# Kernel optimization log

Measured on AMD Instinct MI355X. Metric: run time of the kernel, lower is better.

## Reference

```python
import jax, jax.numpy as jnp
import numpy as np

L = 5  # number of attention+MLP stages

def _layernorm(x, g, b, eps=1e-5):
    mu = x.mean(-1, keepdims=True)
    var = ((x - mu) ** 2).mean(-1, keepdims=True)
    return (x - mu) * jax.lax.rsqrt(var + eps) * g + b

def setup_inputs() -> dict:
    key = jax.random.key(0)
    B, N, C = 8, 2048, 512  # win_size=4, num_slices=12 -> C = 4*4*384//12 = 512
    ks = jax.random.split(key, 7)
    s = 0.02
    return {
        "x": jax.random.normal(ks[0], (B, N, C), dtype=jnp.float32),
        "qkv_w": jax.random.normal(ks[1], (L, C, 3 * C), dtype=jnp.float32) * s,
        "qkv_b": jnp.zeros((L, 3 * C), dtype=jnp.float32),
        "ln_g": jnp.ones((L, C), dtype=jnp.float32),
        "ln_b": jnp.zeros((L, C), dtype=jnp.float32),
        "fc1_w": jax.random.normal(ks[2], (L, C, 2 * C), dtype=jnp.float32) * s,
        "fc1_b": jnp.zeros((L, 2 * C), dtype=jnp.float32),
        "fc2_w": jax.random.normal(ks[3], (L, 2 * C, C), dtype=jnp.float32) * s,
        "fc2_b": jnp.zeros((L, C), dtype=jnp.float32),
    }

def reference(x, qkv_w, qkv_b, ln_g, ln_b, fc1_w, fc1_b, fc2_w, fc2_b):
    B, N, C = x.shape
    half = N // 2
    scale = C ** -0.5  # num_heads = 1 -> head_dim = C
    # Custom block mask: top-left (half x half) block fully visible,
    # top-right block masked; bottom half is tril with diagonal = N//2,
    # i.e. global row i >= half may attend to columns j <= i.
    i = jnp.arange(N)[:, None]
    j = jnp.arange(N)[None, :]
    allowed = jnp.where(i < half, j < half, j <= i)
    bias = jnp.where(allowed, 0.0, -1000.0).astype(x.dtype)  # (N, N)
    for l in range(L):
        # Mask3dAttention (single head)
        qkv = x @ qkv_w[l] + qkv_b[l]                      # (B, N, 3C)
        q, k, v = jnp.split(qkv, 3, axis=-1)               # each (B, N, C)
        attn = jnp.einsum("bnc,bmc->bnm", q * scale, k) + bias
        attn = jax.nn.softmax(attn, axis=-1)
        x = jnp.einsum("bnm,bmc->bnc", attn, v)
        # residual MLP on normed features
        y = _layernorm(x, ln_g[l], ln_b[l])
        h = jax.nn.gelu(y @ fc1_w[l] + fc1_b[l], approximate=False)
        x = x + (h @ fc2_w[l] + fc2_b[l])
    return x
```

## Files before the change

### kernel.cpp

```cpp
#include <hip/hip_runtime.h>
#include <math.h>

typedef unsigned short u16;
typedef __attribute__((ext_vector_type(8))) short bf16x8;
typedef __attribute__((ext_vector_type(4))) float f32x4;
typedef __attribute__((ext_vector_type(4))) unsigned short u16x4;

#define NLAYERS 5
#define BATCH 8
#define SEQ 2048
#define CH 512
#define ROWS_TOTAL (BATCH * SEQ)
#define HALF (SEQ / 2)
#define QSCALE_EXP2 0.06375871529f
#define EXP2_CAP 86.56f

#define SMEM_U16 32768

__device__ __forceinline__ u16 f2bf(float f) {
    unsigned u = __float_as_uint(f);
    u += 0x7fffu + ((u >> 16) & 1u);
    return (u16)(u >> 16);
}

__device__ __forceinline__ unsigned pk2(float a, float b) {
    unsigned r;
    asm("v_cvt_pk_bf16_f32 %0, %1, %2" : "=v"(r) : "v"(a), "v"(b));
    return r;
}

__device__ __forceinline__ u16x4 pack4(f32x4 v) {
    union { unsigned u[2]; u16x4 o; } r;
    r.u[0] = pk2(v[0], v[1]);
    r.u[1] = pk2(v[2], v[3]);
    return r.o;
}

__device__ __forceinline__ void st16(u16* p, u16x4 v) { *(u16x4*)p = v; }
__device__ __forceinline__ void st16f(float* p, f32x4 v) { *(f32x4*)p = v; }

__device__ __forceinline__ float fexp2(float x) {
    float r;
    asm("v_exp_f32 %0, %1" : "=v"(r) : "v"(x));
    return r;
}

__device__ __forceinline__ void llds16(const u16* g, u16* l) {
    __builtin_amdgcn_global_load_lds(
        (const __attribute__((address_space(1))) unsigned int*)g,
        (__attribute__((address_space(3))) unsigned int*)l, 16, 0, 0);
}

__device__ __forceinline__ void xcd_rc(int& rt, int& ct) {
    const int n = blockIdx.x;
    const int m = n >> 3;
    rt = (n & 7) * 16 + (m & 15);
    ct = m >> 4;
}

__device__ __forceinline__ void mm_issue(const u16* gA, const u16* gB,
                                         u16* lA, u16* lB, int lda, int ldb)
{
#pragma unroll
    for (int i = 0; i < 4; ++i)
        llds16(gA + (size_t)i * 32 * lda, lA + i * 2048);
#pragma unroll
    for (int i = 0; i < 4; ++i)
        llds16(gB + (size_t)i * 32 * ldb, lB + i * 2048);
}

__device__ __forceinline__ void mm_compute(const u16* As, const u16* Bs,
                                           const int aoff[2][4],
                                           const int boff[2][4],
                                           f32x4 acc[4][4])
{
#pragma unroll
    for (int h = 0; h < 2; ++h) {
        bf16x8 af[4], bfv[4];
#pragma unroll
        for (int t = 0; t < 4; ++t) af[t]  = *(const bf16x8*)&As[aoff[h][t]];
#pragma unroll
        for (int t = 0; t < 4; ++t) bfv[t] = *(const bf16x8*)&Bs[boff[h][t]];
#pragma unroll
        for (int ti = 0; ti < 4; ++ti)
#pragma unroll
            for (int tj = 0; tj < 4; ++tj)
                acc[ti][tj] = __builtin_amdgcn_mfma_f32_16x16x32_bf16(
                    af[ti], bfv[tj], acc[ti][tj], 0, 0, 0);
    }
}

__device__ __forceinline__ void mm_core(
    const u16* __restrict__ A, int lda,
    const u16* __restrict__ Bt, int ldb,
    int row0, int col0, int K,
    u16* SM, f32x4 acc[4][4])
{
    const int tid  = threadIdx.x;
    const int wave = tid >> 6, lane = tid & 63;
    const int wm = (wave & 1) * 64, wn = (wave >> 1) * 64;
    const int q  = lane >> 4,  ln = lane & 15;

    const int sr8 = lane >> 3;
    const int sc  = (lane & 7) ^ sr8;
    const u16* gA = A  + (size_t)(row0 + wave * 8 + sr8) * lda + sc * 8;
    const u16* gB = Bt + (size_t)(col0 + wave * 8 + sr8) * ldb + sc * 8;

    u16* const A0 = SM;
    u16* const B0 = SM + 8192;
    u16* const A1 = SM + 16384;
    u16* const B1 = SM + 24576;
    u16* const w0a = A0 + wave * 512;
    u16* const w0b = B0 + wave * 512;
    u16* const w1a = A1 + wave * 512;
    u16* const w1b = B1 + wave * 512;

    int aoff[2][4], boff[2][4];
#pragma unroll
    for (int h = 0; h < 2; ++h) {
        const int pos = (((h * 4 + q) ^ (ln & 7)) * 8);
#pragma unroll
        for (int t = 0; t < 4; ++t) {
            aoff[h][t] = (wm + t * 16 + ln) * 64 + pos;
            boff[h][t] = (wn + t * 16 + ln) * 64 + pos;
        }
    }

#pragma unroll
    for (int ti = 0; ti < 4; ++ti)
#pragma unroll
        for (int tj = 0; tj < 4; ++tj)
#pragma unroll
            for (int e = 0; e < 4; ++e) acc[ti][tj][e] = 0.f;

    mm_issue(gA, gB, w0a, w0b, lda, ldb);
    gA += 64; gB += 64;

    for (int k0 = 0; k0 < K; k0 += 128) {
        if (k0 + 64 < K) {
            mm_issue(gA, gB, w1a, w1b, lda, ldb);
            gA += 64; gB += 64;
            asm volatile("s_waitcnt vmcnt(8)" ::: "memory");
        } else {
            asm volatile("s_waitcnt vmcnt(0)" ::: "memory");
        }
        __builtin_amdgcn_s_barrier();
        mm_compute(A0, B0, aoff, boff, acc);
        __builtin_amdgcn_s_barrier();
        __builtin_amdgcn_sched_barrier(0);
        if (k0 + 128 < K) {
            mm_issue(gA, gB, w0a, w0b, lda, ldb);
            gA += 64; gB += 64;
            asm volatile("s_waitcnt vmcnt(8)" ::: "memory");
        } else {
            asm volatile("s_waitcnt vmcnt(0)" ::: "memory");
        }
        __builtin_amdgcn_s_barrier();
        mm_compute(A1, B1, aoff, boff, acc);
        __builtin_amdgcn_s_barrier();
        __builtin_amdgcn_sched_barrier(0);
    }
}

template <typename F>
__device__ __forceinline__ void epi_emit(f32x4 acc[4][4], float* eb, F emit)
{
    const int tid = threadIdx.x, wave = tid >> 6, lane = tid & 63;
    const int wn = (wave >> 1) * 64;
    const int q = lane >> 4, ln = lane & 15;
#pragma unroll
    for (int p = 0; p < 4; ++p) {
        __syncthreads();
        if ((wave & 1) == (p >> 1)) {
            const int tibase = (p & 1) * 2;
#pragma unroll
            for (int tj = 0; tj < 4; ++tj)
#pragma unroll
                for (int t2 = 0; t2 < 2; ++t2)
#pragma unroll
                    for (int r = 0; r < 4; ++r)
                        eb[(t2 * 16 + q * 4 + r) * 132 + wn + tj * 16 + ln] =
                            acc[tibase + t2][tj][r];
        }
        __syncthreads();
#pragma unroll
        for (int s = 0; s < 4; ++s) {
            const int row = s * 8 + (tid >> 5);
            const int col = (tid & 31) * 4;
            f32x4 v = *(const f32x4*)&eb[row * 132 + col];
            emit(p * 32 + row, col, v);
        }
    }
}

__global__ __launch_bounds__(256) void qkv_gemm(
    const u16* __restrict__ A, const u16* __restrict__ Bt,
    const float* __restrict__ bias,
    u16* __restrict__ Qb, u16* __restrict__ Kb, u16* __restrict__ Vt,
    float* __restrict__ rowsum)
{
    __shared__ __align__(16) u16 SMEM[SMEM_U16];
    f32x4 acc[4][4];
    int rt, ct; xcd_rc(rt, ct);
    const int row0 = rt * 128, col0 = ct * 128;
    if (ct == 0 && threadIdx.x < 128)
        rowsum[row0 + threadIdx.x] = 0.f;
    mm_core(A, CH, Bt, CH, row0, col0, CH, SMEM, acc);

    if (ct < 8) {
        u16* dst = (ct < 4) ? Qb : Kb;
        const int cbase = (ct < 4) ? col0 : col0 - CH;
        const float sc = (ct < 4) ? QSCALE_EXP2 : 1.0f;
        epi_emit(acc, (float*)SMEM, [&](int row, int col, f32x4 v) {
            const float4 bb = *(const float4*)&bias[col0 + col];
            v[0] = (v[0] + bb.x) * sc; v[1] = (v[1] + bb.y) * sc;
            v[2] = (v[2] + bb.z) * sc; v[3] = (v[3] + bb.w) * sc;
            st16(&dst[(size_t)(row0 + row) * CH + cbase + col], pack4(v));
        });
    } else {
        const int tid = threadIdx.x, wave = tid >> 6, lane = tid & 63;
        const int wm = (wave & 1) * 64, wn = (wave >> 1) * 64;
        const int q = lane >> 4, ln = lane & 15;
#pragma unroll
        for (int tj = 0; tj < 4; ++tj) {
            const int gcol = col0 + wn + tj * 16 + ln;
            const float bv = bias[gcol];
#pragma unroll
            for (int ti = 0; ti < 4; ++ti) {
                const int grow = row0 + wm + ti * 16 + q * 4;
                const int b = grow >> 11, j = grow & (SEQ - 1);
                f32x4 vv;
                vv[0] = acc[ti][tj][0] + bv; vv[1] = acc[ti][tj][1] + bv;
                vv[2] = acc[ti][tj][2] + bv; vv[3] = acc[ti][tj][3] + bv;
                st16(&Vt[(size_t)b * CH * SEQ +
                         (size_t)(gcol - 2 * CH) * SEQ + j], pack4(vv));
            }
        }
    }
}

__global__ __launch_bounds__(256) void qk_gemm(
    const u16* __restrict__ Qb, const u16* __restrict__ Kb,
    u16* __restrict__ Sb, float* __restrict__ rowsum)
{
    const int id = blockIdx.x;
    const int b = id & 7, jt = (id >> 3) & 15, it = id >> 7;
    if (it < 8) { if (jt >= 8) return; } else if (jt > it) return;
    __shared__ __align__(16) u16 SMEM[SMEM_U16];
    f32x4 acc[4][4];
    const u16* A  = Qb + (size_t)b * SEQ * CH;
    const u16* Bt = Kb + (size_t)b * SEQ * CH;
    u16* S = Sb + (size_t)b * SEQ * SEQ;
    const int row0 = it * 128, col0 = jt * 128;
    mm_core(A, CH, Bt, CH, row0, col0, CH, SMEM, acc);

    const bool upper = (it < 8);
    const int tid = threadIdx.x;
    epi_emit(acc, (float*)SMEM, [&](int row, int col, f32x4 v) {
        const int grow = row0 + row;
        const int gcol = col0 + col;
        f32x4 pv;
#pragma unroll
        for (int e = 0; e < 4; ++e) {
            const bool allowed = upper || (gcol + e <= grow);
            pv[e] = allowed ? fexp2(fminf(v[e], EXP2_CAP)) : 0.f;
        }
        st16(&S[(size_t)grow * SEQ + gcol], pack4(pv));
        float rs = pv[0] + pv[1] + pv[2] + pv[3];
        rs += __shfl_xor(rs, 1, 64);
        rs += __shfl_xor(rs, 2, 64);
        rs += __shfl_xor(rs, 4, 64);
        rs += __shfl_xor(rs, 8, 64);
        rs += __shfl_xor(rs, 16, 64);
        if ((tid & 31) == 0)
            atomicAdd(&rowsum[b * SEQ + grow], rs);
    });
}

__global__ __launch_bounds__(256) void pv_gemm(
    const u16* __restrict__ Sb, const u16* __restrict__ Vt,
    const float* __restrict__ rowsum, float* __restrict__ O)
{
    const int n = blockIdx.x;
    const int b = n & 7, m = n >> 3;
    const int it = 15 - (m >> 2), ct = m & 3;
    const int Kfull = ((it < 8) ? 8 : (it + 1)) * 128;
    __shared__ __align__(16) u16 SMEM[SMEM_U16];
    f32x4 acc[4][4];
    const u16* A  = Sb + (size_t)b * SEQ * SEQ;
    const u16* Bt = Vt + (size_t)b * CH * SEQ;
    const int row0 = it * 128, col0 = ct * 128;
    mm_core(A, SEQ, Bt, SEQ, row0, col0, Kfull, SMEM, acc);

    epi_emit(acc, (float*)SMEM, [&](int row, int col, f32x4 v) {
        const int grow = row0 + row;
        const float rden = 1.0f / rowsum[b * SEQ + grow];
        v[0] *= rden; v[1] *= rden; v[2] *= rden; v[3] *= rden;
        st16f(&O[(size_t)(b * SEQ + grow) * CH + col0 + col], v);
    });
}

__global__ __launch_bounds__(256) void fc1_gemm(
    const u16* __restrict__ A, const u16* __restrict__ Bt,
    const float* __restrict__ bias, u16* __restrict__ H)
{
    __shared__ __align__(16) u16 SMEM[SMEM_U16];
    f32x4 acc[4][4];
    int rt, ct; xcd_rc(rt, ct);
    const int row0 = rt * 128, col0 = ct * 128;
    mm_core(A, CH, Bt, CH, row0, col0, CH, SMEM, acc);
    epi_emit(acc, (float*)SMEM, [&](int row, int col, f32x4 v) {
        const float4 bb = *(const float4*)&bias[col0 + col];
        v[0] += bb.x; v[1] += bb.y; v[2] += bb.z; v[3] += bb.w;
#pragma unroll
        for (int e = 0; e < 4; ++e)
            v[e] = 0.5f * v[e] * (1.f + erff(v[e] * 0.70710678118654752f));
        st16(&H[(size_t)(row0 + row) * (2 * CH) + col0 + col], pack4(v));
    });
}

template <bool WRITE_X>
__global__ __launch_bounds__(256) void fc2_gemm(
    const u16* __restrict__ A, const u16* __restrict__ Bt,
    const float* __restrict__ bias, float* __restrict__ X,
    u16* __restrict__ Xb)
{
    __shared__ __align__(16) u16 SMEM[SMEM_U16];
    f32x4 acc[4][4];
    int rt, ct; xcd_rc(rt, ct);
    const int row0 = rt * 128, col0 = ct * 128;
    mm_core(A, 2 * CH, Bt, 2 * CH, row0, col0, 2 * CH, SMEM, acc);
    epi_emit(acc, (float*)SMEM, [&](int row, int col, f32x4 v) {
        const size_t idx = (size_t)(row0 + row) * CH + col0 + col;
        const float4 bb = *(const float4*)&bias[col0 + col];
        const f32x4 xv = *(const f32x4*)&X[idx];
        v[0] += bb.x + xv[0]; v[1] += bb.y + xv[1];
        v[2] += bb.z + xv[2]; v[3] += bb.w + xv[3];
        if (WRITE_X) st16f(&X[idx], v);
        st16(&Xb[idx], pack4(v));
    });
}

__device__ __forceinline__ float block_sum(float v, volatile float* red, int tid)
{
#pragma unroll
    for (int off = 1; off < 64; off <<= 1) v += __shfl_xor(v, off, 64);
    __syncthreads();
    if ((tid & 63) == 0) red[tid >> 6] = v;
    __syncthreads();
    return red[0] + red[1] + red[2] + red[3];
}

__global__ __launch_bounds__(256) void ln_kernel(
    const float* __restrict__ x, const float* __restrict__ g,
    const float* __restrict__ bta, u16* __restrict__ y)
{
    __shared__ float red[4];
    const int tid = threadIdx.x;
    const size_t base = (size_t)blockIdx.x * CH;
    float x0 = x[base + tid];
    float x1 = x[base + 256 + tid];
    float mu = block_sum(x0 + x1, red, tid) * (1.f / CH);
    float d0 = x0 - mu, d1 = x1 - mu;
    float var = block_sum(d0 * d0 + d1 * d1, red, tid) * (1.f / CH);
    float w = 1.f / sqrtf(var + 1e-5f);
    const float y0 = d0 * w * g[tid]       + bta[tid];
    const float y1 = d1 * w * g[256 + tid] + bta[256 + tid];
    const unsigned pk = pk2(y0, y1);
    y[base + tid]       = (u16)(pk & 0xffffu);
    y[base + 256 + tid] = (u16)(pk >> 16);
}

__global__ __launch_bounds__(256) void f2bf_kernel(
    const float* __restrict__ in, u16* __restrict__ out)
{
    const int i = blockIdx.x * 256 + threadIdx.x;
    float4 vv = ((const float4*)in)[i];
    f32x4 v; v[0] = vv.x; v[1] = vv.y; v[2] = vv.z; v[3] = vv.w;
    u16x4 o = pack4(v);
    *(u16x4*)&out[(size_t)i * 4] = o;
}

__global__ __launch_bounds__(256) void wtrans_kernel(
    const float* __restrict__ in, u16* __restrict__ out, int K, int N)
{
    __shared__ float tile[32][33];
    const int l = blockIdx.z;
    in  += (size_t)l * K * N;
    out += (size_t)l * K * N;
    const int n0 = blockIdx.x * 32, k0 = blockIdx.y * 32;
    const int r = threadIdx.x >> 3, c4 = (threadIdx.x & 7) * 4;
    float4 v = *(const float4*)&in[(size_t)(k0 + r) * N + n0 + c4];
    tile[r][c4 + 0] = v.x; tile[r][c4 + 1] = v.y;
    tile[r][c4 + 2] = v.z; tile[r][c4 + 3] = v.w;
    __syncthreads();
    f32x4 t;
    t[0] = tile[c4 + 0][r]; t[1] = tile[c4 + 1][r];
    t[2] = tile[c4 + 2][r]; t[3] = tile[c4 + 3][r];
    st16(&out[(size_t)(n0 + r) * K + k0 + c4], pack4(t));
}

extern "C" void kernel_launch(void* const* d_in, const int* in_sizes, int n_in,
                              void* d_out, int out_size, void* d_ws, size_t ws_size,
                              hipStream_t stream)
{
    const float* x_in  = (const float*)d_in[0];
    const float* qkv_w = (const float*)d_in[1];
    const float* qkv_b = (const float*)d_in[2];
    const float* ln_g  = (const float*)d_in[3];
    const float* ln_b  = (const float*)d_in[4];
    const float* fc1_w = (const float*)d_in[5];
    const float* fc1_b = (const float*)d_in[6];
    const float* fc2_w = (const float*)d_in[7];
    const float* fc2_b = (const float*)d_in[8];

    float* xbuf = (float*)d_out;

    char* p = (char*)d_ws;
    u16* qkv_wt = (u16*)p; p += (size_t)NLAYERS * 1536 * 512 * 2;
    u16* fc1_wt = (u16*)p; p += (size_t)NLAYERS * 1024 * 512 * 2;
    u16* fc2_wt = (u16*)p; p += (size_t)NLAYERS * 512 * 1024 * 2;
    u16* xb = (u16*)p; p += (size_t)ROWS_TOTAL * CH * 2;
    u16* Qb = (u16*)p; p += (size_t)ROWS_TOTAL * CH * 2;
    u16* Kb = (u16*)p; p += (size_t)ROWS_TOTAL * CH * 2;
    u16* Vt = (u16*)p; p += (size_t)ROWS_TOTAL * CH * 2;
    float* rowsum = (float*)p; p += (size_t)ROWS_TOTAL * 4;
    u16* Sb = (u16*)p;
    u16* yb = Sb;
    u16* hb = Sb + (size_t)ROWS_TOTAL * CH;

    const dim3 blk(256);

    f2bf_kernel<<<dim3(ROWS_TOTAL * CH / 1024), blk, 0, stream>>>(x_in, xb);
    wtrans_kernel<<<dim3(1536 / 32, 512 / 32, NLAYERS), blk, 0, stream>>>(
        qkv_w, qkv_wt, 512, 1536);
    wtrans_kernel<<<dim3(1024 / 32, 512 / 32, NLAYERS), blk, 0, stream>>>(
        fc1_w, fc1_wt, 512, 1024);
    wtrans_kernel<<<dim3(512 / 32, 1024 / 32, NLAYERS), blk, 0, stream>>>(
        fc2_w, fc2_wt, 1024, 512);

    for (int l = 0; l < NLAYERS; ++l) {
        qkv_gemm<<<dim3(128 * 12), blk, 0, stream>>>(
            xb, qkv_wt + (size_t)l * 1536 * 512, qkv_b + (size_t)l * 1536,
            Qb, Kb, Vt, rowsum);
        qk_gemm<<<dim3(2048), blk, 0, stream>>>(Qb, Kb, Sb, rowsum);
        pv_gemm<<<dim3(512), blk, 0, stream>>>(Sb, Vt, rowsum, xbuf);
        ln_kernel<<<dim3(ROWS_TOTAL), blk, 0, stream>>>(
            xbuf, ln_g + (size_t)l * CH, ln_b + (size_t)l * CH, yb);
        fc1_gemm<<<dim3(128 * 8), blk, 0, stream>>>(
            yb, fc1_wt + (size_t)l * 1024 * 512, fc1_b + (size_t)l * 1024, hb);
        if (l < NLAYERS - 1)
            fc2_gemm<false><<<dim3(128 * 4), blk, 0, stream>>>(
                hb, fc2_wt + (size_t)l * 512 * 1024, fc2_b + (size_t)l * 512,
                xbuf, xb);
        else
            fc2_gemm<true><<<dim3(128 * 4), blk, 0, stream>>>(
                hb, fc2_wt + (size_t)l * 512 * 1024, fc2_b + (size_t)l * 512,
                xbuf, xb);
    }
}
```

Baseline: 1.045 ms.

## Retile QK^T GEMM to 128x256 tiles with 512 threads and compact grid

Replaces the QK score kernel with a 512-thread variant computing 128x256 output tiles, so each Q tile load is reused across twice as many key columns. The grid is compacted to enumerate only the needed tiles of the block-causal mask instead of launching 2048 blocks and early-exiting most of them. The epilogue is staged through shared memory in four 32-row passes to fit the smaller LDS budget, with a full-wave rowsum reduction. Some tiles at the causal boundary now cover partially masked columns, which adds wasted work there, and the larger block with 4 blocks per CU may raise register pressure.

Measured after the change: 980.5 us. 6.2% less time.

```diff
diff --git a/kernel.cpp b/kernel.cpp
--- a/kernel.cpp
+++ b/kernel.cpp
@@ -16,6 +16,7 @@
 #define EXP2_CAP 86.56f
 
 #define SMEM_U16 32768
+#define QK2_U16 24576
 
 __device__ __forceinline__ u16 f2bf(float f) {
     unsigned u = __float_as_uint(f);
@@ -239,42 +240,116 @@
     }
 }
 
-__global__ __launch_bounds__(256) void qk_gemm(
+__global__ __launch_bounds__(512, 4) void qk2_gemm(
     const u16* __restrict__ Qb, const u16* __restrict__ Kb,
     u16* __restrict__ Sb, float* __restrict__ rowsum)
 {
+    __shared__ __align__(16) u16 SMEM[QK2_U16];
+    u16* const As = SMEM;
+    u16* const Bs = SMEM + 8192;
+    float* const eb = (float*)SMEM;
+
     const int id = blockIdx.x;
-    const int b = id & 7, jt = (id >> 3) & 15, it = id >> 7;
-    if (it < 8) { if (jt >= 8) return; } else if (jt > it) return;
-    __shared__ __align__(16) u16 SMEM[SMEM_U16];
+    const int b = id & 7;
+    int u = id >> 3, it, pr;
+    if (u < 32) { it = u >> 2; pr = u & 3; }
+    else {
+        int v = u - 32; it = 8; int len = 5;
+        while (v >= len) { v -= len; ++it; len = 5 + ((it - 8) >> 1); }
+        pr = v;
+    }
+
+    const int tid = threadIdx.x;
+    const int w = tid >> 6, lane = tid & 63;
+    const int wq = w & 3;
+    const int wm = (wq & 1) * 64;
+    const int wn = (w >> 2) * 128 + (wq >> 1) * 64;
+    const int q = lane >> 4, ln = lane & 15;
+    const int sr8 = lane >> 3, sc = (lane & 7) ^ sr8;
+
+    const int row0 = it * 128, col0 = pr * 256;
+    const u16* const Qg = Qb + (size_t)b * SEQ * CH;
+    const u16* const Kg = Kb + (size_t)b * SEQ * CH;
+    u16* const S = Sb + (size_t)b * SEQ * SEQ;
+
+    const u16* gA = Qg + (size_t)(row0 + w * 16 + sr8) * CH + sc * 8;
+    const u16* gB = Kg + (size_t)(col0 + w * 32 + sr8) * CH + sc * 8;
+    u16* const lA = As + w * 1024;
+    u16* const lB = Bs + w * 2048;
+
+    int aoff[2][4], boff[2][4];
+#pragma unroll
+    for (int h = 0; h < 2; ++h) {
+        const int pos = (((h * 4 + q) ^ (ln & 7)) * 8);
+#pragma unroll
+        for (int t = 0; t < 4; ++t) {
+            aoff[h][t] = (wm + t * 16 + ln) * 64 + pos;
+            boff[h][t] = (wn + t * 16 + ln) * 64 + pos;
+        }
+    }
+
     f32x4 acc[4][4];
-    const u16* A  = Qb + (size_t)b * SEQ * CH;
-    const u16* Bt = Kb + (size_t)b * SEQ * CH;
-    u16* S = Sb + (size_t)b * SEQ * SEQ;
-    const int row0 = it * 128, col0 = jt * 128;
-    mm_core(A, CH, Bt, CH, row0, col0, CH, SMEM, acc);
+#pragma unroll
+    for (int ti = 0; ti < 4; ++ti)
+#pragma unroll
+        for (int tj = 0; tj < 4; ++tj)
+#pragma unroll
+            for (int e = 0; e < 4; ++e) acc[ti][tj][e] = 0.f;
+
+    for (int s = 0; s < 8; ++s) {
+        __syncthreads();
+        llds16(gA,               lA);
+        llds16(gA +  8 * CH,     lA + 512);
+        llds16(gB,               lB);
+        llds16(gB +  8 * CH,     lB + 512);
+        llds16(gB + 16 * CH,     lB + 1024);
+        llds16(gB + 24 * CH,     lB + 1536);
+        gA += 64; gB += 64;
+        __syncthreads();
+        mm_compute(As, Bs, aoff, boff, acc);
+    }
 
     const bool upper = (it < 8);
-    const int tid = threadIdx.x;
-    epi_emit(acc, (float*)SMEM, [&](int row, int col, f32x4 v) {
-        const int grow = row0 + row;
-        const int gcol = col0 + col;
-        f32x4 pv;
-#pragma unroll
-        for (int e = 0; e < 4; ++e) {
-            const bool allowed = upper || (gcol + e <= grow);
-            pv[e] = allowed ? fexp2(fminf(v[e], EXP2_CAP)) : 0.f;
-        }
-        st16(&S[(size_t)grow * SEQ + gcol], pack4(pv));
-        float rs = pv[0] + pv[1] + pv[2] + pv[3];
-        rs += __shfl_xor(rs, 1, 64);
-        rs += __shfl_xor(rs, 2, 64);
-        rs += __shfl_xor(rs, 4, 64);
-        rs += __shfl_xor(rs, 8, 64);
-        rs += __shfl_xor(rs, 16, 64);
-        if ((tid & 31) == 0)
-            atomicAdd(&rowsum[b * SEQ + grow], rs);
-    });
+#pragma unroll
+    for (int p = 0; p < 4; ++p) {
+        __syncthreads();
+        if ((wq & 1) == (p >> 1)) {
+            const int tibase = (p & 1) * 2;
+#pragma unroll
+            for (int tj = 0; tj < 4; ++tj)
+#pragma unroll
+                for (int t2 = 0; t2 < 2; ++t2)
+#pragma unroll
+                    for (int r = 0; r < 4; ++r)
+                        eb[(t2 * 16 + q * 4 + r) * 260 + wn + tj * 16 + ln] =
+                            acc[tibase + t2][tj][r];
+        }
+        __syncthreads();
+#pragma unroll
+        for (int s2 = 0; s2 < 4; ++s2) {
+            const int row = s2 * 8 + w;
+            const int col = lane * 4;
+            f32x4 v = *(const f32x4*)&eb[row * 260 + col];
+            const int grow = row0 + p * 32 + row;
+            const int gcol = col0 + col;
+            f32x4 pv;
+#pragma unroll
+            for (int e = 0; e < 4; ++e) {
+                const bool allowed = upper || (gcol + e <= grow);
+                pv[e] = allowed ? fexp2(fminf(v[e], EXP2_CAP)) : 0.f;
+            }
+            st16(&S[(size_t)grow * SEQ + gcol], pack4(pv));
+            float rs = pv[0] + pv[1] + pv[2] + pv[3];
+            rs += __shfl_xor(rs, 1, 64);
+            rs += __shfl_xor(rs, 2, 64);
+            rs += __shfl_xor(rs, 4, 64);
+            rs += __shfl_xor(rs, 8, 64);
+            rs += __shfl_xor(rs, 16, 64);
+            rs += __shfl_xor(rs, 32, 64);
+            if (lane == 0)
+                atomicAdd(&rowsum[b * SEQ + grow], rs);
+        }
+    }
 }
 
 __global__ __launch_bounds__(256) void pv_gemm(
@@ -430,6 +505,7 @@
     u16* hb = Sb + (size_t)ROWS_TOTAL * CH;
 
     const dim3 blk(256);
+    const dim3 blk2(512);
 
     f2bf_kernel<<<dim3(ROWS_TOTAL * CH / 1024), blk, 0, stream>>>(x_in, xb);
     wtrans_kernel<<<dim3(1536 / 32, 512 / 32, NLAYERS), blk, 0, stream>>>(
@@ -443,7 +519,7 @@
         qkv_gemm<<<dim3(128 * 12), blk, 0, stream>>>(
             xb, qkv_wt + (size_t)l * 1536 * 512, qkv_b + (size_t)l * 1536,
             Qb, Kb, Vt, rowsum);
-        qk_gemm<<<dim3(2048), blk, 0, stream>>>(Qb, Kb, Sb, rowsum);
+        qk2_gemm<<<dim3(672), blk2, 0, stream>>>(Qb, Kb, Sb, rowsum);
         pv_gemm<<<dim3(512), blk, 0, stream>>>(Sb, Vt, rowsum, xbuf);
         ln_kernel<<<dim3(ROWS_TOTAL), blk, 0, stream>>>(
             xbuf, ln_g + (size_t)l * CH, ln_b + (size_t)l * CH, yb);
```
